# Performance work log

Hardware: AMD Instinct MI355X
Metric: run time of the kernel (lower is better)

Reference implementation:

```python
import jax, jax.numpy as jnp
import numpy as np

D_MODEL = 2048
N_HEADS = 16
N_KV = 4
D_HEAD = 128
D1 = 64
D2 = 64
WSIZE = 1024
EPS = 1e-6
ROPE_BASE = 10000.0


def _rmsnorm(x):
    # RMSNorm over last dim, no affine weight
    return x * jax.lax.rsqrt(jnp.mean(x * x, axis=-1, keepdims=True) + EPS)


def _apply_rope(x, cos, sin):
    # x: (..., D2); cos/sin: (1, T, 1, D2//2)
    h = D2 // 2
    x1, x2 = x[..., :h], x[..., h:]
    return jnp.concatenate([x1 * cos + x2 * sin, -x1 * sin + x2 * cos], axis=-1)


def setup_inputs() -> dict:
    key = jax.random.key(0)
    ks = jax.random.split(key, 6)
    B, T = 2, 2048
    return {
        "hidden_states": jax.random.normal(ks[0], (B, T, D_MODEL), dtype=jnp.float32),
        "W_qkv": jax.random.normal(ks[1], (D_MODEL, (N_HEADS + N_KV) * D_HEAD), dtype=jnp.float32) * 0.02,
        "W_rk": jax.random.normal(ks[2], (D_MODEL, D2), dtype=jnp.float32) * 0.02,
        "b_rk": jax.random.normal(ks[3], (D2,), dtype=jnp.float32) * 0.02,
        "softmax_scaler": jnp.ones((N_HEADS,), dtype=jnp.float32),
        "W_g": jax.random.normal(ks[5], (D_MODEL, D_MODEL), dtype=jnp.float32) * 0.02,
    }


def reference(hidden_states, W_qkv, W_rk, b_rk, softmax_scaler, W_g):
    x = hidden_states
    B, T, _ = x.shape
    # fused qkv projection + per-(head,token) RMSNorm (qk_norm)
    qkv = (x @ W_qkv).reshape(B, T, N_HEADS + N_KV, D_HEAD)
    qkv = _rmsnorm(qkv)
    q, kv = qkv[:, :, :N_HEADS], qkv[:, :, N_HEADS:]
    q_nope, q_rope = q[..., :D1], q[..., D1:]

    # head-tied rope key: shared across all heads
    k_rope = (x @ W_rk + b_rk)[:, :, None, :]  # (B, T, 1, D2)

    # rotary embedding (start_pos = 0)
    inv_freq = 1.0 / (ROPE_BASE ** (jnp.arange(0, D2, 2, dtype=jnp.float32) / D2))
    freqs = jnp.arange(T, dtype=jnp.float32)[:, None] * inv_freq[None, :]  # (T, D2//2)
    cos = jnp.cos(freqs)[None, :, None, :]
    sin = jnp.sin(freqs)[None, :, None, :]
    q_rope = _apply_rope(q_rope, cos, sin)
    k_rope = jnp.broadcast_to(_apply_rope(k_rope, cos, sin), (B, T, N_HEADS, D2))

    q = jnp.concatenate([q_nope, q_rope], axis=-1)  # (B, T, H, D_HEAD)

    # scalable softmax: scale q by per-head scaler * log(min(pos, wsize))
    pos = jnp.arange(1, T + 1, dtype=jnp.float32)
    log_pos = jnp.log(jnp.minimum(pos, float(WSIZE)))[None, :, None, None]
    q = softmax_scaler[None, None, :, None] * log_pos * q

    # tied k/v: first D1 of kv shared between k and v; repeat kv heads (GQA)
    kv_tied, v = kv[..., :D1], kv[..., D1:]
    rep = N_HEADS // N_KV
    kv_tied = jnp.repeat(kv_tied, rep, axis=2)  # (B, T, H, D1)
    v = jnp.repeat(v, rep, axis=2)              # (B, T, H, D2)
    k = jnp.concatenate([kv_tied, k_rope], axis=-1)   # (B, T, H, D_HEAD)
    v_full = jnp.concatenate([kv_tied, v], axis=-1)   # (B, T, H, D_HEAD)

    # sliding-window causal attention: key j valid iff i - WSIZE <= j <= i
    scores = jnp.einsum('bthd,bshd->bhts', q, k) / np.float32(np.sqrt(D_HEAD))
    i = jnp.arange(T)[:, None]
    j = jnp.arange(T)[None, :]
    mask = (j <= i) & (j >= i - WSIZE)
    scores = jnp.where(mask[None, None], scores, jnp.float32(-1e30))
    p = jax.nn.softmax(scores, axis=-1)
    y = jnp.einsum('bhts,bshd->bthd', p, v_full)  # (B, T, H, D_HEAD)

    # elementwise silu gate
    g = (x @ W_g).reshape(B, T, N_HEADS, D_HEAD)
    return y * jax.nn.silu(g)
```

## Files before the change

kernel.cpp:

```cpp
#include <hip/hip_runtime.h>

typedef _Float16 f16;
typedef _Float16 half8 __attribute__((ext_vector_type(8)));
typedef _Float16 half4_t __attribute__((ext_vector_type(4)));
typedef float f32x4 __attribute__((ext_vector_type(4)));

#define T_SEQ 2048
#define B_SZ 2
#define DM 2048
#define NH 16
#define NKV 4
#define DH 128
#define NQKV 2560
#define NALL 4736
#define NALLP 4864
#define COL_RK 2560
#define COL_G 2688
#define M_ROWS 4096
#define WIN 1024

typedef __attribute__((address_space(1))) const unsigned int guint;
typedef __attribute__((address_space(3))) unsigned int luint;
__device__ __forceinline__ void gload16(const void* g, void* l) {
  __builtin_amdgcn_global_load_lds((guint*)g, (luint*)l, 16, 0, 0);
}

__global__ void k_cvt(const float* __restrict__ in, f16* __restrict__ out, int n) {
  int i = (blockIdx.x * 256 + threadIdx.x) * 4;
  if (i >= n) return;
  float4 v = *(const float4*)(in + i);
  half4_t o;
  o[0] = (f16)v.x; o[1] = (f16)v.y; o[2] = (f16)v.z; o[3] = (f16)v.w;
  *(half4_t*)(out + i) = o;
}

__global__ __launch_bounds__(256) void k_cvt_t(const float* __restrict__ W,
                                               f16* __restrict__ Wt, int K, int N) {
  __shared__ float tile[32][33];
  int k0 = blockIdx.x * 32, n0 = blockIdx.y * 32;
  int tx = threadIdx.x & 31, ty = threadIdx.x >> 5;
#pragma unroll
  for (int r = 0; r < 32; r += 8)
    tile[ty + r][tx] = W[(size_t)(k0 + ty + r) * N + n0 + tx];
  __syncthreads();
#pragma unroll
  for (int r = 0; r < 32; r += 8)
    Wt[(size_t)(n0 + ty + r) * K + k0 + tx] = (f16)tile[tx][ty + r];
}

__global__ __launch_bounds__(256) void k_vt(const f16* __restrict__ v, f16* __restrict__ vt) {
  __shared__ f16 tile[32][34];
  int t0 = blockIdx.x * 32, d0 = blockIdx.y * 32, m = blockIdx.z;
  int tx = threadIdx.x & 31, ty = threadIdx.x >> 5;
  const f16* src = v + (size_t)m * T_SEQ * DH;
  f16* dst = vt + (size_t)m * T_SEQ * DH;
#pragma unroll
  for (int r = 0; r < 32; r += 8)
    tile[ty + r][tx] = src[(size_t)(t0 + ty + r) * DH + d0 + tx];
  __syncthreads();
#pragma unroll
  for (int r = 0; r < 32; r += 8)
    dst[(size_t)(d0 + ty + r) * T_SEQ + t0 + tx] = tile[tx][ty + r];
}

#define GEMM_PHASE3(cb, sb, nt)                                                             \
  {                                                                                         \
    char* Ab = lds + (cb) * 16384;                                                          \
    char* Bb = lds + 49152 + (cb) * 8192;                                                   \
    int koff = (nt) * 32;                                                                   \
    half8 af[4], bf[4];                                                                     \
    _Pragma("unroll")                                                                       \
    for (int i = 0; i < 4; ++i)                                                             \
      af[i] = *(const half8*)(Ab + (wm * 64 + i * 16 + fr) * 64 + xsl);                     \
    _Pragma("unroll")                                                                       \
    for (int j = 0; j < 4; ++j)                                                             \
      bf[j] = *(const half8*)(Bb + (wn * 64 + j * 16 + fr) * 64 + xsl);                     \
    gload16(Ag0 + koff, lds + (sb) * 16384 + w * 1024);                                     \
    gload16(Ag1 + koff, lds + (sb) * 16384 + 8192 + w * 1024);                              \
    gload16(Bg + koff, lds + 49152 + (sb) * 8192 + w * 1024);                               \
    __builtin_amdgcn_s_barrier();                                                           \
    __builtin_amdgcn_sched_barrier(0);                                                      \
    asm volatile("s_waitcnt lgkmcnt(0)" ::: "memory");                                      \
    __builtin_amdgcn_sched_barrier(0);                                                      \
    __builtin_amdgcn_s_setprio(1);                                                          \
    _Pragma("unroll")                                                                       \
    for (int i = 0; i < 4; ++i)                                                             \
      _Pragma("unroll")                                                                     \
      for (int j = 0; j < 4; ++j)                                                           \
        acc[i][j] = __builtin_amdgcn_mfma_f32_16x16x32_f16(af[i], bf[j], acc[i][j], 0, 0, 0); \
    __builtin_amdgcn_s_setprio(0);                                                          \
    asm volatile("s_waitcnt vmcnt(3)" ::: "memory");                                        \
    __builtin_amdgcn_s_barrier();                                                           \
    __builtin_amdgcn_sched_barrier(0);                                                      \
  }

__global__ __launch_bounds__(512, 4) void k_gemm8(const f16* __restrict__ A,
                                                  const f16* __restrict__ Bt,
                                                  f16* __restrict__ C) {
  __shared__ __align__(16) char lds[73728];
  const int K = DM;
  unsigned orig = blockIdx.y * 38u + blockIdx.x;
  unsigned swz = (orig & 7u) * 76u + (orig >> 3);
  int m0 = (int)(swz / 38u) * 256;
  int n0 = (int)(swz % 38u) * 128;
  int tid = threadIdx.x, lane = tid & 63, w = tid >> 6;
  int wm = w >> 1, wn = w & 1;
  int fr = lane & 15, fq = lane >> 4;
  int xsl = (fq ^ ((fr >> 1) & 3)) << 4;
  int sr = tid >> 2, ss = tid & 3;
  int scol = (ss ^ ((sr >> 1) & 3)) * 8;
  f32x4 acc[4][4] = {};
  const f16* Ag0 = A + (size_t)(m0 + sr) * K + scol;
  const f16* Ag1 = A + (size_t)(m0 + 128 + sr) * K + scol;
  const f16* Bg  = Bt + (size_t)(n0 + sr) * K + scol;

  gload16(Ag0, lds + w * 1024);
  gload16(Ag1, lds + 8192 + w * 1024);
  gload16(Bg, lds + 49152 + w * 1024);
  gload16(Ag0 + 32, lds + 16384 + w * 1024);
  gload16(Ag1 + 32, lds + 16384 + 8192 + w * 1024);
  gload16(Bg + 32, lds + 49152 + 8192 + w * 1024);
  asm volatile("s_waitcnt vmcnt(3)" ::: "memory");
  __builtin_amdgcn_s_barrier();
  __builtin_amdgcn_sched_barrier(0);

#pragma unroll 1
  for (int t3 = 0; t3 < 21; ++t3) {
    int ktb = t3 * 3;
    int n1_ = ktb + 3 <= 63 ? ktb + 3 : 63;
    int n2_ = ktb + 4 <= 63 ? ktb + 4 : 63;
    GEMM_PHASE3(0, 2, ktb + 2);
    GEMM_PHASE3(1, 0, n1_);
    GEMM_PHASE3(2, 1, n2_);
  }
  GEMM_PHASE3(0, 2, 63);

#pragma unroll
  for (int i = 0; i < 4; ++i) {
    int row = m0 + wm * 64 + i * 16 + fq * 4;
#pragma unroll
    for (int j = 0; j < 4; ++j) {
      int col = n0 + wn * 64 + j * 16 + fr;
      f16* Cp = C + (size_t)row * NALLP + col;
#pragma unroll
      for (int rr = 0; rr < 4; ++rr) Cp[(size_t)rr * NALLP] = (f16)acc[i][j][rr];
    }
  }
}

__global__ __launch_bounds__(256) void k_postproc(
    const f16* __restrict__ CA,
    const float* __restrict__ brk, const float* __restrict__ sscal,
    f16* __restrict__ q16, f16* __restrict__ k16, f16* __restrict__ v16) {
  int row = blockIdx.x;
  int b = row >> 11, t = row & 2047;
  int lane = threadIdx.x & 63, wid = threadIdx.x >> 6;
  int ridx = lane & 31;
  float inv_freq = exp2f(-(float)ridx * 0.41524101186092074f);
  float fr = (float)t * inv_freq;
  float cs = cosf(fr), sn = sinf(fr);
  float logpos = 0.6931471805599453f * __log2f(fminf((float)(t + 1), 1024.0f));
  const float rsqrt_d_log2e = 0.08838834764831845f * 1.4426950408889634f;
  const f16* Crow = CA + (size_t)row * NALLP;
#pragma unroll
  for (int p = 0; p < 5; ++p) {
    int h = p * 4 + wid;
    float v0 = (float)Crow[h * 128 + lane];
    float v1 = (float)Crow[h * 128 + 64 + lane];
    float ss = v0 * v0 + v1 * v1;
#pragma unroll
    for (int m = 1; m < 64; m <<= 1) ss += __shfl_xor(ss, m);
    float rms = rsqrtf(ss * (1.0f / 128.0f) + 1e-6f);
    v0 *= rms; v1 *= rms;
    if (h < NH) {
      float part = __shfl_xor(v1, 32);
      float vr = (lane < 32) ? (v1 * cs + part * sn) : (v1 * cs - part * sn);
      float scale = sscal[h] * logpos * rsqrt_d_log2e;
      size_t qb = ((size_t)(b * NH + h) * T_SEQ + t) * DH;
      q16[qb + lane]      = (f16)(v0 * scale);
      q16[qb + 64 + lane] = (f16)(vr * scale);
    } else {
      int hk = h - NH;
      size_t kb = ((size_t)(b * NKV + hk) * T_SEQ + t) * DH;
      k16[kb + lane]      = (f16)v0;
      v16[kb + lane]      = (f16)v0;
      v16[kb + 64 + lane] = (f16)v1;
    }
  }
  if (wid == 0) {
    float kr = (float)Crow[COL_RK + lane] + brk[lane];
    float part = __shfl_xor(kr, 32);
    float vr = (lane < 32) ? (kr * cs + part * sn) : (kr * cs - part * sn);
    f16 hv = (f16)vr;
#pragma unroll
    for (int hk = 0; hk < NKV; ++hk)
      k16[((size_t)(b * NKV + hk) * T_SEQ + t) * DH + 64 + lane] = hv;
  }
}

__global__ __launch_bounds__(256, 2) void k_attn(
    const f16* __restrict__ q16, const f16* __restrict__ k16, const f16* __restrict__ vt16,
    const f16* __restrict__ gA, float* __restrict__ out) {
  __shared__ __align__(16) char lds[40960];
  int bx = blockIdx.x;
  int qt = (bx & 1) ? (31 - (bx >> 1)) : (bx >> 1);
  int h = blockIdx.y, b = blockIdx.z, hk = h >> 2;
  int tid = threadIdx.x, lane = tid & 63, w = tid >> 6;
  int i0 = qt * 64, iw = i0 + w * 16;
  int fr = lane & 15, fq = lane >> 4;

  char* Psb = lds + 32768 + w * 2048;

  const f16* qbase = q16 + ((size_t)(b * NH + h) * T_SEQ + iw + fr) * DH;
  half8 qf[4];
#pragma unroll
  for (int kb = 0; kb < 4; ++kb) qf[kb] = *(const half8*)&qbase[kb * 32 + fq * 8];

  f32x4 o[8] = {};
  float mrow[4] = {-1e30f, -1e30f, -1e30f, -1e30f};
  float lrow[4] = {0.f, 0.f, 0.f, 0.f};

  const f16* kg = k16 + (size_t)(b * NKV + hk) * T_SEQ * DH;
  const f16* vg = vt16 + (size_t)(b * NKV + hk) * T_SEQ * DH;

  int jt0 = qt >= 16 ? qt - 16 : 0;

  for (int jt = jt0; jt <= qt; ++jt) {
    int j0 = jt * 64;
#pragma unroll
    for (int i = 0; i < 4; ++i) {
      int r = i * 16 + (tid >> 4);
      int c = ((tid & 15) ^ (r & 7)) * 8;
      gload16(kg + (size_t)(j0 + r) * DH + c, lds + i * 4096 + w * 1024);
    }
#pragma unroll
    for (int i = 0; i < 4; ++i) {
      int r = i * 32 + (tid >> 3);
      int c = ((tid & 7) ^ (r & 7)) * 8;
      gload16(vg + (size_t)r * T_SEQ + j0 + c, lds + 16384 + i * 4096 + w * 1024);
    }
    asm volatile("s_waitcnt vmcnt(0)" ::: "memory");
    __syncthreads();

    f32x4 s[4] = {};
    __builtin_amdgcn_s_setprio(1);
#pragma unroll
    for (int nf = 0; nf < 4; ++nf) {
      int row = nf * 16 + fr;
      int sw = fr & 7;
#pragma unroll
      for (int kb = 0; kb < 4; ++kb) {
        half8 bfv = *(const half8*)(lds + row * 256 + ((((kb << 2) | fq) ^ sw) << 4));
        s[nf] = __builtin_amdgcn_mfma_f32_16x16x32_f16(qf[kb], bfv, s[nf], 0, 0, 0);
      }
    }
    __builtin_amdgcn_s_setprio(0);
    int il = (w << 4) + (fq << 2);
    if (jt == qt) {
#pragma unroll
      for (int nf = 0; nf < 4; ++nf) {
        int jo = nf * 16 + fr;
#pragma unroll
        for (int r = 0; r < 4; ++r)
          if (jo > il + r) s[nf][r] = -3e38f;
      }
    } else if (qt >= 16 && jt == jt0) {
#pragma unroll
      for (int nf = 0; nf < 4; ++nf) {
        int jo = nf * 16 + fr;
#pragma unroll
        for (int r = 0; r < 4; ++r)
          if (jo < il + r) s[nf][r] = -3e38f;
      }
    }
    float tm[4];
#pragma unroll
    for (int r = 0; r < 4; ++r)
      tm[r] = fmaxf(fmaxf(s[0][r], s[1][r]), fmaxf(s[2][r], s[3][r]));
#pragma unroll
    for (int r = 0; r < 4; ++r) {
      tm[r] = fmaxf(tm[r], __shfl_xor(tm[r], 1));
      tm[r] = fmaxf(tm[r], __shfl_xor(tm[r], 2));
      tm[r] = fmaxf(tm[r], __shfl_xor(tm[r], 4));
      tm[r] = fmaxf(tm[r], __shfl_xor(tm[r], 8));
    }
    bool need = false;
#pragma unroll
    for (int r = 0; r < 4; ++r) need = need || (tm[r] > mrow[r] + 8.0f);
    if (__any(need)) {
#pragma unroll
      for (int r = 0; r < 4; ++r) {
        float mn = fmaxf(mrow[r], tm[r]);
        float sc = exp2f(mrow[r] - mn);
        mrow[r] = mn;
        lrow[r] *= sc;
#pragma unroll
        for (int of = 0; of < 8; ++of) o[of][r] *= sc;
      }
    }
    float ls[4] = {0.f, 0.f, 0.f, 0.f};
#pragma unroll
    for (int nf = 0; nf < 4; ++nf)
#pragma unroll
      for (int r = 0; r < 4; ++r) {
        float pv = exp2f(s[nf][r] - mrow[r]);
        s[nf][r] = pv;
        ls[r] += pv;
      }
#pragma unroll
    for (int r = 0; r < 4; ++r) {
      float t2 = ls[r];
      t2 += __shfl_xor(t2, 1); t2 += __shfl_xor(t2, 2);
      t2 += __shfl_xor(t2, 4); t2 += __shfl_xor(t2, 8);
      lrow[r] += t2;
    }
#pragma unroll
    for (int nf = 0; nf < 4; ++nf) {
      int sbase = (nf << 1) + (fr >> 3);
      int boff = (fr & 7) << 1;
#pragma unroll
      for (int r = 0; r < 4; ++r) {
        int q = (fq << 2) + r;
        *(f16*)(Psb + q * 128 + ((sbase ^ (q & 7)) << 4) + boff) = (f16)s[nf][r];
      }
    }
    asm volatile("s_waitcnt lgkmcnt(0)" ::: "memory");
    __builtin_amdgcn_sched_barrier(0);
    half8 pf0 = *(const half8*)(Psb + fr * 128 + (((fq) ^ (fr & 7)) << 4));
    half8 pf1 = *(const half8*)(Psb + fr * 128 + (((4 | fq) ^ (fr & 7)) << 4));
    __builtin_amdgcn_s_setprio(1);
#pragma unroll
    for (int of = 0; of < 8; ++of) {
      int vrow0 = of * 16 + fr;
      int sw = fr & 7;
      half8 v0 = *(const half8*)(lds + 16384 + vrow0 * 128 + ((fq ^ sw) << 4));
      half8 v1 = *(const half8*)(lds + 16384 + vrow0 * 128 + (((4 | fq) ^ sw) << 4));
      o[of] = __builtin_amdgcn_mfma_f32_16x16x32_f16(pf0, v0, o[of], 0, 0, 0);
      o[of] = __builtin_amdgcn_mfma_f32_16x16x32_f16(pf1, v1, o[of], 0, 0, 0);
    }
    __builtin_amdgcn_s_setprio(0);
    __syncthreads();
  }
  const f16* gb = gA + ((size_t)(b * T_SEQ) + iw) * NALLP + COL_G + h * DH;
  float* ob = out + ((size_t)(b * T_SEQ) + iw) * DM + h * DH;
#pragma unroll
  for (int r = 0; r < 4; ++r) {
    float inv = 1.0f / lrow[r];
    int ir = fq * 4 + r;
#pragma unroll
    for (int of = 0; of < 8; ++of) {
      int d = of * 16 + fr;
      float gv = (float)gb[(size_t)ir * NALLP + d];
      float sig = gv / (1.0f + expf(-gv));
      ob[(size_t)ir * DM + d] = o[of][r] * inv * sig;
    }
  }
}

extern "C" void kernel_launch(void* const* d_in, const int* in_sizes, int n_in,
                              void* d_out, int out_size, void* d_ws, size_t ws_size,
                              hipStream_t stream) {
  const float* x     = (const float*)d_in[0];
  const float* Wqkv  = (const float*)d_in[1];
  const float* Wrk   = (const float*)d_in[2];
  const float* brk   = (const float*)d_in[3];
  const float* sscal = (const float*)d_in[4];
  const float* Wg    = (const float*)d_in[5];
  float* out = (float*)d_out;
  char* ws = (char*)d_ws;
  size_t off = 0;
  auto alloc = [&](size_t bytes) -> void* {
    void* p = ws + off;
    off += (bytes + 255) & ~(size_t)255;
    return p;
  };
  f16* x16     = (f16*)alloc((size_t)M_ROWS * DM * 2);
  f16* BtAll   = (f16*)alloc((size_t)NALLP * DM * 2);
  f16* CAll    = (f16*)alloc((size_t)M_ROWS * NALLP * 2);
  f16* q16     = (f16*)alloc((size_t)B_SZ * NH * T_SEQ * DH * 2);
  f16* k16     = (f16*)alloc((size_t)B_SZ * NKV * T_SEQ * DH * 2);
  f16* v16     = (f16*)alloc((size_t)B_SZ * NKV * T_SEQ * DH * 2);
  f16* vt16    = (f16*)alloc((size_t)B_SZ * NKV * T_SEQ * DH * 2);

  k_cvt<<<(M_ROWS * DM / 4 + 255) / 256, 256, 0, stream>>>(x, x16, M_ROWS * DM);
  k_cvt_t<<<dim3(DM / 32, NQKV / 32), 256, 0, stream>>>(Wqkv, BtAll, DM, NQKV);
  k_cvt_t<<<dim3(DM / 32, 64 / 32), 256, 0, stream>>>(Wrk, BtAll + (size_t)COL_RK * DM, DM, 64);
  k_cvt_t<<<dim3(DM / 32, DM / 32), 256, 0, stream>>>(Wg, BtAll + (size_t)COL_G * DM, DM, DM);

  k_gemm8<<<dim3(NALLP / 128, M_ROWS / 256), 512, 0, stream>>>(x16, BtAll, CAll);

  k_postproc<<<M_ROWS, 256, 0, stream>>>(CAll, brk, sscal, q16, k16, v16);
  k_vt<<<dim3(T_SEQ / 32, DH / 32, B_SZ * NKV), 256, 0, stream>>>(v16, vt16);

  k_attn<<<dim3(T_SEQ / 64, NH, B_SZ), 256, 0, stream>>>(q16, k16, vt16, CAll, out);
}
```

Before: 338.7 us.

## Enlarge per-wave GEMM tiles and transpose attention scores to column-per-query layout

The fused projection GEMM drops from 512 to 256 threads per block, so each wave now computes a 128x64 output tile in two phases, reusing its B fragments across both phases and interleaving the global-to-LDS loads. This raises MFMA work per LDS read but raises register use and lowers the thread count per block. The attention kernel swaps the MFMA operand order so each lane owns one query row, which turns the per-row max and sum reductions into two cross-lane shuffles. P is then written to LDS as packed half4 stores instead of scalar stores.

After: 304.9 us. 1.11x faster.

```diff
diff --git a/kernel.cpp b/kernel.cpp
--- a/kernel.cpp
+++ b/kernel.cpp
@@ -63,42 +63,55 @@
     dst[(size_t)(d0 + ty + r) * T_SEQ + t0 + tx] = tile[tx][ty + r];
 }
 
-#define GEMM_PHASE3(cb, sb, nt)                                                             \
-  {                                                                                         \
-    char* Ab = lds + (cb) * 16384;                                                          \
-    char* Bb = lds + 49152 + (cb) * 8192;                                                   \
-    int koff = (nt) * 32;                                                                   \
-    half8 af[4], bf[4];                                                                     \
-    _Pragma("unroll")                                                                       \
-    for (int i = 0; i < 4; ++i)                                                             \
-      af[i] = *(const half8*)(Ab + (wm * 64 + i * 16 + fr) * 64 + xsl);                     \
-    _Pragma("unroll")                                                                       \
-    for (int j = 0; j < 4; ++j)                                                             \
-      bf[j] = *(const half8*)(Bb + (wn * 64 + j * 16 + fr) * 64 + xsl);                     \
-    gload16(Ag0 + koff, lds + (sb) * 16384 + w * 1024);                                     \
-    gload16(Ag1 + koff, lds + (sb) * 16384 + 8192 + w * 1024);                              \
-    gload16(Bg + koff, lds + 49152 + (sb) * 8192 + w * 1024);                               \
-    __builtin_amdgcn_s_barrier();                                                           \
-    __builtin_amdgcn_sched_barrier(0);                                                      \
-    asm volatile("s_waitcnt lgkmcnt(0)" ::: "memory");                                      \
-    __builtin_amdgcn_sched_barrier(0);                                                      \
-    __builtin_amdgcn_s_setprio(1);                                                          \
-    _Pragma("unroll")                                                                       \
-    for (int i = 0; i < 4; ++i)                                                             \
-      _Pragma("unroll")                                                                     \
-      for (int j = 0; j < 4; ++j)                                                           \
-        acc[i][j] = __builtin_amdgcn_mfma_f32_16x16x32_f16(af[i], bf[j], acc[i][j], 0, 0, 0); \
-    __builtin_amdgcn_s_setprio(0);                                                          \
-    asm volatile("s_waitcnt vmcnt(3)" ::: "memory");                                        \
-    __builtin_amdgcn_s_barrier();                                                           \
-    __builtin_amdgcn_sched_barrier(0);                                                      \
-  }
-
-__global__ __launch_bounds__(512, 4) void k_gemm8(const f16* __restrict__ A,
+#define GEMM_PHASE(cb, sb, nt, ph)                                                     \
+  {                                                                                    \
+    char* Ab = lds + (cb) * 24576;                                                     \
+    char* Bb = lds + (cb) * 24576 + 16384;                                             \
+    half8 af[4];                                                                       \
+    _Pragma("unroll")                                                                  \
+    for (int i = 0; i < 4; ++i)                                                        \
+      af[i] = *(const half8*)(Ab + (wm * 128 + (ph) * 64 + i * 16 + fr) * 64 + xsl);   \
+    if ((ph) == 0) {                                                                   \
+      _Pragma("unroll")                                                                \
+      for (int j = 0; j < 4; ++j)                                                      \
+        bfr[j] = *(const half8*)(Bb + (wn * 64 + j * 16 + fr) * 64 + xsl);             \
+    }                                                                                  \
+    {                                                                                  \
+      char* Sb = lds + (sb) * 24576;                                                   \
+      int koff = (nt) * 32;                                                            \
+      if ((ph) == 0) {                                                                 \
+        gload16(Ag + koff, Sb + tid * 16);                                             \
+        gload16(Ag + (size_t)64 * DM + koff, Sb + 4096 + tid * 16);                    \
+        gload16(Ag + (size_t)128 * DM + koff, Sb + 8192 + tid * 16);                   \
+      } else {                                                                         \
+        gload16(Ag + (size_t)192 * DM + koff, Sb + 12288 + tid * 16);                  \
+        gload16(Bg + koff, Sb + 16384 + tid * 16);                                     \
+        gload16(Bg + (size_t)64 * DM + koff, Sb + 20480 + tid * 16);                   \
+      }                                                                                \
+    }                                                                                  \
+    __builtin_amdgcn_s_barrier();                                                      \
+    __builtin_amdgcn_sched_barrier(0);                                                 \
+    asm volatile("s_waitcnt lgkmcnt(0)" ::: "memory");                                 \
+    __builtin_amdgcn_sched_barrier(0);                                                 \
+    __builtin_amdgcn_s_setprio(1);                                                     \
+    _Pragma("unroll")                                                                  \
+    for (int i = 0; i < 4; ++i)                                                        \
+      _Pragma("unroll")                                                                \
+      for (int j = 0; j < 4; ++j)                                                      \
+        acc[(ph) * 4 + i][j] = __builtin_amdgcn_mfma_f32_16x16x32_f16(                 \
+            af[i], bfr[j], acc[(ph) * 4 + i][j], 0, 0, 0);                             \
+    __builtin_amdgcn_s_setprio(0);                                                     \
+    if ((ph) == 1) asm volatile("s_waitcnt vmcnt(6)" ::: "memory");                    \
+    __builtin_amdgcn_s_barrier();                                                      \
+    __builtin_amdgcn_sched_barrier(0);                                                 \
+  }
+
+#define GEMM_KT(cb, sb, nt) GEMM_PHASE(cb, sb, nt, 0) GEMM_PHASE(cb, sb, nt, 1)
+
+__global__ __launch_bounds__(256, 2) void k_gemm8(const f16* __restrict__ A,
                                                   const f16* __restrict__ Bt,
                                                   f16* __restrict__ C) {
   __shared__ __align__(16) char lds[73728];
-  const int K = DM;
   unsigned orig = blockIdx.y * 38u + blockIdx.x;
   unsigned swz = (orig & 7u) * 76u + (orig >> 3);
   int m0 = (int)(swz / 38u) * 256;
@@ -107,43 +120,47 @@
   int wm = w >> 1, wn = w & 1;
   int fr = lane & 15, fq = lane >> 4;
   int xsl = (fq ^ ((fr >> 1) & 3)) << 4;
-  int sr = tid >> 2, ss = tid & 3;
-  int scol = (ss ^ ((sr >> 1) & 3)) * 8;
-  f32x4 acc[4][4] = {};
-  const f16* Ag0 = A + (size_t)(m0 + sr) * K + scol;
-  const f16* Ag1 = A + (size_t)(m0 + 128 + sr) * K + scol;
-  const f16* Bg  = Bt + (size_t)(n0 + sr) * K + scol;
-
-  gload16(Ag0, lds + w * 1024);
-  gload16(Ag1, lds + 8192 + w * 1024);
-  gload16(Bg, lds + 49152 + w * 1024);
-  gload16(Ag0 + 32, lds + 16384 + w * 1024);
-  gload16(Ag1 + 32, lds + 16384 + 8192 + w * 1024);
-  gload16(Bg + 32, lds + 49152 + 8192 + w * 1024);
-  asm volatile("s_waitcnt vmcnt(3)" ::: "memory");
+  int scol = ((tid & 3) ^ ((tid >> 3) & 3)) * 8;
+  f32x4 acc[8][4] = {};
+  half8 bfr[4];
+  const f16* Ag = A + (size_t)(m0 + (tid >> 2)) * DM + scol;
+  const f16* Bg = Bt + (size_t)(n0 + (tid >> 2)) * DM + scol;
+
+  gload16(Ag, lds + tid * 16);
+  gload16(Ag + (size_t)64 * DM, lds + 4096 + tid * 16);
+  gload16(Ag + (size_t)128 * DM, lds + 8192 + tid * 16);
+  gload16(Ag + (size_t)192 * DM, lds + 12288 + tid * 16);
+  gload16(Bg, lds + 16384 + tid * 16);
+  gload16(Bg + (size_t)64 * DM, lds + 20480 + tid * 16);
+  gload16(Ag + 32, lds + 24576 + tid * 16);
+  gload16(Ag + (size_t)64 * DM + 32, lds + 24576 + 4096 + tid * 16);
+  gload16(Ag + (size_t)128 * DM + 32, lds + 24576 + 8192 + tid * 16);
+  gload16(Ag + (size_t)192 * DM + 32, lds + 24576 + 12288 + tid * 16);
+  gload16(Bg + 32, lds + 24576 + 16384 + tid * 16);
+  gload16(Bg + (size_t)64 * DM + 32, lds + 24576 + 20480 + tid * 16);
+  asm volatile("s_waitcnt vmcnt(6)" ::: "memory");
   __builtin_amdgcn_s_barrier();
   __builtin_amdgcn_sched_barrier(0);
 
 #pragma unroll 1
   for (int t3 = 0; t3 < 21; ++t3) {
-    int ktb = t3 * 3;
-    int n1_ = ktb + 3 <= 63 ? ktb + 3 : 63;
-    int n2_ = ktb + 4 <= 63 ? ktb + 4 : 63;
-    GEMM_PHASE3(0, 2, ktb + 2);
-    GEMM_PHASE3(1, 0, n1_);
-    GEMM_PHASE3(2, 1, n2_);
-  }
-  GEMM_PHASE3(0, 2, 63);
-
-#pragma unroll
-  for (int i = 0; i < 4; ++i) {
-    int row = m0 + wm * 64 + i * 16 + fq * 4;
+    int kb0 = t3 * 3;
+    int n3 = kb0 + 4 <= 63 ? kb0 + 4 : 63;
+    GEMM_KT(0, 2, kb0 + 2);
+    GEMM_KT(1, 0, kb0 + 3);
+    GEMM_KT(2, 1, n3);
+  }
+  GEMM_KT(0, 2, 63);
+
+#pragma unroll
+  for (int ii = 0; ii < 8; ++ii) {
+    int row = m0 + wm * 128 + (ii >> 2) * 64 + (ii & 3) * 16 + fq * 4;
 #pragma unroll
     for (int j = 0; j < 4; ++j) {
       int col = n0 + wn * 64 + j * 16 + fr;
       f16* Cp = C + (size_t)row * NALLP + col;
 #pragma unroll
-      for (int rr = 0; rr < 4; ++rr) Cp[(size_t)rr * NALLP] = (f16)acc[i][j][rr];
+      for (int rr = 0; rr < 4; ++rr) Cp[(size_t)rr * NALLP] = (f16)acc[ii][j][rr];
     }
   }
 }
@@ -217,8 +234,7 @@
   for (int kb = 0; kb < 4; ++kb) qf[kb] = *(const half8*)&qbase[kb * 32 + fq * 8];
 
   f32x4 o[8] = {};
-  float mrow[4] = {-1e30f, -1e30f, -1e30f, -1e30f};
-  float lrow[4] = {0.f, 0.f, 0.f, 0.f};
+  float mrow = -1e30f, lrow = 0.f;
 
   const f16* kg = k16 + (size_t)(b * NKV + hk) * T_SEQ * DH;
   const f16* vg = vt16 + (size_t)(b * NKV + hk) * T_SEQ * DH;
@@ -250,79 +266,70 @@
       int sw = fr & 7;
 #pragma unroll
       for (int kb = 0; kb < 4; ++kb) {
-        half8 bfv = *(const half8*)(lds + row * 256 + ((((kb << 2) | fq) ^ sw) << 4));
-        s[nf] = __builtin_amdgcn_mfma_f32_16x16x32_f16(qf[kb], bfv, s[nf], 0, 0, 0);
+        half8 kfv = *(const half8*)(lds + row * 256 + ((((kb << 2) | fq) ^ sw) << 4));
+        s[nf] = __builtin_amdgcn_mfma_f32_16x16x32_f16(kfv, qf[kb], s[nf], 0, 0, 0);
       }
     }
     __builtin_amdgcn_s_setprio(0);
-    int il = (w << 4) + (fq << 2);
+    int ql = (w << 4) + fr;
     if (jt == qt) {
 #pragma unroll
       for (int nf = 0; nf < 4; ++nf) {
-        int jo = nf * 16 + fr;
+        int kbase = nf * 16 + (fq << 2);
 #pragma unroll
         for (int r = 0; r < 4; ++r)
-          if (jo > il + r) s[nf][r] = -3e38f;
+          if (kbase + r > ql) s[nf][r] = -3e38f;
       }
     } else if (qt >= 16 && jt == jt0) {
 #pragma unroll
       for (int nf = 0; nf < 4; ++nf) {
-        int jo = nf * 16 + fr;
+        int kbase = nf * 16 + (fq << 2);
 #pragma unroll
         for (int r = 0; r < 4; ++r)
-          if (jo < il + r) s[nf][r] = -3e38f;
+          if (kbase + r < ql) s[nf][r] = -3e38f;
       }
     }
-    float tm[4];
-#pragma unroll
-    for (int r = 0; r < 4; ++r)
-      tm[r] = fmaxf(fmaxf(s[0][r], s[1][r]), fmaxf(s[2][r], s[3][r]));
-#pragma unroll
-    for (int r = 0; r < 4; ++r) {
-      tm[r] = fmaxf(tm[r], __shfl_xor(tm[r], 1));
-      tm[r] = fmaxf(tm[r], __shfl_xor(tm[r], 2));
-      tm[r] = fmaxf(tm[r], __shfl_xor(tm[r], 4));
-      tm[r] = fmaxf(tm[r], __shfl_xor(tm[r], 8));
-    }
-    bool need = false;
-#pragma unroll
-    for (int r = 0; r < 4; ++r) need = need || (tm[r] > mrow[r] + 8.0f);
-    if (__any(need)) {
-#pragma unroll
-      for (int r = 0; r < 4; ++r) {
-        float mn = fmaxf(mrow[r], tm[r]);
-        float sc = exp2f(mrow[r] - mn);
-        mrow[r] = mn;
-        lrow[r] *= sc;
-#pragma unroll
-        for (int of = 0; of < 8; ++of) o[of][r] *= sc;
+    float a0 = fmaxf(fmaxf(s[0][0], s[0][1]), fmaxf(s[0][2], s[0][3]));
+    float a1 = fmaxf(fmaxf(s[1][0], s[1][1]), fmaxf(s[1][2], s[1][3]));
+    float a2 = fmaxf(fmaxf(s[2][0], s[2][1]), fmaxf(s[2][2], s[2][3]));
+    float a3 = fmaxf(fmaxf(s[3][0], s[3][1]), fmaxf(s[3][2], s[3][3]));
+    float tm = fmaxf(fmaxf(a0, a1), fmaxf(a2, a3));
+    tm = fmaxf(tm, __shfl_xor(tm, 16));
+    tm = fmaxf(tm, __shfl_xor(tm, 32));
+    if (__any(tm > mrow + 8.0f)) {
+      float mn = fmaxf(mrow, tm);
+      float sc = exp2f(mrow - mn);
+      mrow = mn;
+      lrow *= sc;
+      float s0 = __shfl(sc, (fq << 2) + 0);
+      float s1 = __shfl(sc, (fq << 2) + 1);
+      float s2 = __shfl(sc, (fq << 2) + 2);
+      float s3 = __shfl(sc, (fq << 2) + 3);
+#pragma unroll
+      for (int of = 0; of < 8; ++of) {
+        o[of][0] *= s0; o[of][1] *= s1; o[of][2] *= s2; o[of][3] *= s3;
       }
     }
-    float ls[4] = {0.f, 0.f, 0.f, 0.f};
 #pragma unroll
     for (int nf = 0; nf < 4; ++nf)
 #pragma unroll
-      for (int r = 0; r < 4; ++r) {
-        float pv = exp2f(s[nf][r] - mrow[r]);
-        s[nf][r] = pv;
-        ls[r] += pv;
-      }
-#pragma unroll
-    for (int r = 0; r < 4; ++r) {
-      float t2 = ls[r];
-      t2 += __shfl_xor(t2, 1); t2 += __shfl_xor(t2, 2);
-      t2 += __shfl_xor(t2, 4); t2 += __shfl_xor(t2, 8);
-      lrow[r] += t2;
-    }
+      for (int r = 0; r < 4; ++r)
+        s[nf][r] = exp2f(s[nf][r] - mrow);
+    float l0 = (s[0][0] + s[0][1]) + (s[0][2] + s[0][3]);
+    float l1 = (s[1][0] + s[1][1]) + (s[1][2] + s[1][3]);
+    float l2 = (s[2][0] + s[2][1]) + (s[2][2] + s[2][3]);
+    float l3 = (s[3][0] + s[3][1]) + (s[3][2] + s[3][3]);
+    float ls = (l0 + l1) + (l2 + l3);
+    ls += __shfl_xor(ls, 16);
+    ls += __shfl_xor(ls, 32);
+    lrow += ls;
 #pragma unroll
     for (int nf = 0; nf < 4; ++nf) {
-      int sbase = (nf << 1) + (fr >> 3);
-      int boff = (fr & 7) << 1;
-#pragma unroll
-      for (int r = 0; r < 4; ++r) {
-        int q = (fq << 2) + r;
-        *(f16*)(Psb + q * 128 + ((sbase ^ (q & 7)) << 4) + boff) = (f16)s[nf][r];
-      }
+      half4_t p4;
+      p4[0] = (f16)s[nf][0]; p4[1] = (f16)s[nf][1];
+      p4[2] = (f16)s[nf][2]; p4[3] = (f16)s[nf][3];
+      int sl = ((nf << 1) + (fq >> 1)) ^ (fr & 7);
+      *(half4_t*)(Psb + fr * 128 + (sl << 4) + ((fq & 1) << 3)) = p4;
     }
     asm volatile("s_waitcnt lgkmcnt(0)" ::: "memory");
     __builtin_amdgcn_sched_barrier(0);
@@ -341,18 +348,23 @@
     __builtin_amdgcn_s_setprio(0);
     __syncthreads();
   }
+  float rinv = 1.0f / lrow;
+  float iv0 = __shfl(rinv, (fq << 2) + 0);
+  float iv1 = __shfl(rinv, (fq << 2) + 1);
+  float iv2 = __shfl(rinv, (fq << 2) + 2);
+  float iv3 = __shfl(rinv, (fq << 2) + 3);
+  float ivv[4] = {iv0, iv1, iv2, iv3};
   const f16* gb = gA + ((size_t)(b * T_SEQ) + iw) * NALLP + COL_G + h * DH;
   float* ob = out + ((size_t)(b * T_SEQ) + iw) * DM + h * DH;
 #pragma unroll
   for (int r = 0; r < 4; ++r) {
-    float inv = 1.0f / lrow[r];
     int ir = fq * 4 + r;
 #pragma unroll
     for (int of = 0; of < 8; ++of) {
       int d = of * 16 + fr;
       float gv = (float)gb[(size_t)ir * NALLP + d];
       float sig = gv / (1.0f + expf(-gv));
-      ob[(size_t)ir * DM + d] = o[of][r] * inv * sig;
+      ob[(size_t)ir * DM + d] = o[of][r] * ivv[r] * sig;
     }
   }
 }
@@ -387,7 +399,7 @@
   k_cvt_t<<<dim3(DM / 32, 64 / 32), 256, 0, stream>>>(Wrk, BtAll + (size_t)COL_RK * DM, DM, 64);
   k_cvt_t<<<dim3(DM / 32, DM / 32), 256, 0, stream>>>(Wg, BtAll + (size_t)COL_G * DM, DM, DM);
 
-  k_gemm8<<<dim3(NALLP / 128, M_ROWS / 256), 512, 0, stream>>>(x16, BtAll, CAll);
+  k_gemm8<<<dim3(38, 16), 256, 0, stream>>>(x16, BtAll, CAll);
 
   k_postproc<<<M_ROWS, 256, 0, stream>>>(CAll, brk, sscal, q16, k16, v16);
   k_vt<<<dim3(T_SEQ / 32, DH / 32, B_SZ * NKV), 256, 0, stream>>>(v16, vt16);
```
